# Kernel optimization log

Measured on AMD Instinct MI355X. Metric: run time of the kernel, lower is better.

Reference implementation:

```python
import jax, jax.numpy as jnp
import numpy as np

D, B, V = 8, 4096, 1024          # token fields (type..section), batch streams, vocab per field
THRES = 0.9                      # top_k filter_thres default
TEMP = 1.0                       # temperature default
NOTE_TYPE = 1                    # note_type_code; sos=0, eos=2


def setup_inputs() -> dict:
    key = jax.random.key(0)
    k1, k2, k3 = jax.random.split(key, 3)
    logits = jax.random.normal(k1, (D, B, V), dtype=jnp.float32)
    u = jax.random.uniform(k2, (D, B, V), dtype=jnp.float32)
    current_values = jax.random.randint(k3, (D, B), 0, 16).astype(jnp.int32)
    return {"logits": logits, "u": u, "current_values": current_values}


def reference(logits, u, current_values):
    neg = -jnp.inf
    ar = jnp.arange(V)
    # monotonicity mask: positions < current value are forbidden  [D,B,V]
    lg = jnp.where(ar[None, None, :] < current_values[:, :, None], neg, logits)
    # index 0 is masked for every field (logits[d][:, 0] = -inf in the loop)
    lg = lg.at[:, :, 0].set(neg)
    # top-k filtering: keep values >= k-th largest, k = int((1 - thres) * V)
    k = int((1.0 - THRES) * V)
    kth = jax.lax.top_k(lg, k)[0][..., -1:]          # [D,B,1]
    filt = jnp.where(lg < kth, neg, lg)
    logp = jax.nn.log_softmax(filt / TEMP, axis=-1)  # stable softmax, -inf -> prob 0
    probs = jnp.exp(logp)
    # multinomial sampling via Gumbel-max using provided uniform noise
    eps = 1e-20
    gumbel = -jnp.log(-jnp.log(u + eps) + eps)
    samples = jnp.argmax(logp + gumbel, axis=-1)     # [D,B]
    # type-conditional fill: fields 1..7 are zero unless sampled type == NOTE
    is_note = samples[0] == NOTE_TYPE                # [B]
    keep = (jnp.arange(D)[:, None] == 0) | is_note[None, :]
    tokens = jnp.where(keep, samples, 0)             # [D,B]
    return tokens.T, probs                           # [B,D] int, [D,B,V] float
```

## Files before the change

kernel.cpp:

```cpp
#include <hip/hip_runtime.h>
#include <math.h>

#define DD 8
#define BB 4096
#define VV 1024
#define K_SEL 102
#define RPB 4

typedef float vf4 __attribute__((ext_vector_type(4)));

__device__ __forceinline__ unsigned f2key(float f) {
    unsigned u = __float_as_uint(f);
    unsigned m = (unsigned)((int)u >> 31) | 0x80000000u;
    return u ^ m;
}
__device__ __forceinline__ float key2f(unsigned k) {
    unsigned m = 0x80000000u | ~((unsigned)((int)k >> 31));
    return __uint_as_float(k ^ m);
}

__global__ __launch_bounds__(256, 8) void decode_row_kernel(
    const float* __restrict__ logits,
    const float* __restrict__ unoise,
    const int* __restrict__ curvals,
    float* __restrict__ probs_out,
    int* __restrict__ samples)
{
    const int wave = threadIdx.x >> 6;
    const int lane = threadIdx.x & 63;
    const int row  = blockIdx.x * RPB + wave;

    const vf4* l4 = (const vf4*)(logits + (size_t)row * VV);
    const vf4* u4 = (const vf4*)(unoise + (size_t)row * VV);
    const int cv1 = max(curvals[row], 1);

    vf4 lf[4];
#pragma unroll
    for (int i = 0; i < 4; i++) lf[i] = l4[i * 64 + lane];
    vf4 uu[4];
#pragma unroll
    for (int i = 0; i < 4; i++) uu[i] = __builtin_nontemporal_load(&u4[i * 64 + lane]);

    unsigned key[16];
    {
        const int vb = lane * 4;
#pragma unroll
        for (int j = 0; j < 4; j++) {
            float t = (vb + j < cv1) ? -INFINITY : lf[0][j];
            key[j] = f2key(t);
        }
    }
#pragma unroll
    for (int i = 1; i < 4; i++)
#pragma unroll
        for (int j = 0; j < 4; j++)
            key[i * 4 + j] = f2key(lf[i][j]);
    if (cv1 > 256) {
#pragma unroll
        for (int i = 1; i < 4; i++)
#pragma unroll
            for (int j = 0; j < 4; j++)
                if (i * 256 + lane * 4 + j < cv1) key[i * 4 + j] = f2key(-INFINITY);
    }

    unsigned p  = 0u;
    unsigned CA = 0u;
#pragma unroll
    for (int b = 30; b >= 16; b -= 2) {
        const unsigned t1 = p + (1u << b);
        const unsigned t2 = p + (2u << b);
        const unsigned t3 = p + (3u << b);
        unsigned c1 = 0, c2 = 0, c3 = 0;
#pragma unroll
        for (int i = 0; i < 16; i++) {
            c1 += (unsigned)__popcll(__ballot(key[i] >= t1));
            c2 += (unsigned)__popcll(__ballot(key[i] >= t2));
            c3 += (unsigned)__popcll(__ballot(key[i] >= t3));
        }
        if (c3 >= K_SEL)      { p = t3; }
        else if (c2 >= K_SEL) { p = t2; CA = c3; }
        else if (c1 >= K_SEL) { p = t1; CA = c2; }
        else                  {         CA = c1; }
    }
    unsigned kk = K_SEL - CA;

    unsigned cmask = 0u;
#pragma unroll
    for (int i = 0; i < 16; i++)
        if ((key[i] & 0xFFFF0000u) == p) cmask |= (1u << i);
    unsigned thr;
    for (;;) {
        unsigned mx = 0u;
#pragma unroll
        for (int i = 0; i < 16; i++)
            if (cmask & (1u << i)) mx = max(mx, key[i]);
#pragma unroll
        for (int off = 32; off; off >>= 1)
            mx = max(mx, (unsigned)__shfl_xor((int)mx, off, 64));
        if (kk <= 1u) { thr = mx; break; }
        unsigned ceq = 0u;
#pragma unroll
        for (int i = 0; i < 16; i++)
            ceq += (unsigned)__popcll(__ballot(key[i] == mx));
        if (kk <= ceq) { thr = mx; break; }
        kk -= ceq;
#pragma unroll
        for (int i = 0; i < 16; i++)
            if (key[i] == mx) cmask &= ~(1u << i);
    }

    float ex[16];
    float s = 0.0f;
#pragma unroll
    for (int i = 0; i < 16; i++) {
        float e = (key[i] >= thr) ? __expf(key2f(key[i])) : 0.0f;
        ex[i] = e;
        s += e;
    }
#pragma unroll
    for (int off = 32; off; off >>= 1)
        s += __shfl_xor(s, off, 64);
    const float inv = 1.0f / s;

    float bnum = 0.0f, bden = 1.0f;
    int   besti = VV;
    vf4* p4 = (vf4*)(probs_out + (size_t)row * VV);
#pragma unroll
    for (int i = 0; i < 4; i++) {
        vf4 pv;
        pv.x = ex[i * 4 + 0] * inv;
        pv.y = ex[i * 4 + 1] * inv;
        pv.z = ex[i * 4 + 2] * inv;
        pv.w = ex[i * 4 + 3] * inv;
        p4[i * 64 + lane] = pv;
#pragma unroll
        for (int j = 0; j < 4; j++) {
            const int idx = i * 4 + j;
            float nl = 1e-20f - __logf(uu[i][j] + 1e-20f);
            float a  = ex[idx];
            int v = i * 256 + lane * 4 + j;
            if (a * bden > bnum * nl) { bnum = a; bden = nl; besti = v; }
        }
    }
#pragma unroll
    for (int off = 32; off; off >>= 1) {
        float onum = __shfl_xor(bnum, off, 64);
        float oden = __shfl_xor(bden, off, 64);
        int   oi   = __shfl_xor(besti, off, 64);
        float x = onum * bden, y = bnum * oden;
        if (x > y || (x == y && oi < besti)) { bnum = onum; bden = oden; besti = oi; }
    }
    if (lane == 0) samples[row] = besti;
}

__global__ __launch_bounds__(256) void tokens_kernel(
    const int* __restrict__ samples, float* __restrict__ tokens_out)
{
    int i = blockIdx.x * 256 + threadIdx.x;
    int b = i >> 3;
    int d = i & 7;
    int sm = samples[d * BB + b];
    int t0 = samples[b];
    tokens_out[i] = (d == 0 || t0 == 1) ? (float)sm : 0.0f;
}

extern "C" void kernel_launch(void* const* d_in, const int* in_sizes, int n_in,
                              void* d_out, int out_size, void* d_ws, size_t ws_size,
                              hipStream_t stream) {
    const float* logits = (const float*)d_in[0];
    const float* unoise = (const float*)d_in[1];
    const int*   curvals = (const int*)d_in[2];

    float* out        = (float*)d_out;
    float* tokens_out = out;
    float* probs_out  = out + (size_t)BB * DD;
    int*   samples    = (int*)d_ws;

    decode_row_kernel<<<(DD * BB) / RPB, 256, 0, stream>>>(logits, unoise, curvals,
                                                           probs_out, samples);
    tokens_kernel<<<(BB * DD) / 256, 256, 0, stream>>>(samples, tokens_out);
}
```

Before: 313.4 us.

## Radix-select on float compares with data-informed starting bucket

Replaces the unsigned key transform with direct float comparisons against thresholds decoded from key-space pivots, which drops the per-element key conversion. It also adds a speculative first pass that counts elements at or above 0.5 and 2.0. When the k-th largest value falls in that range, the select starts from a known prefix, which skips the early radix rounds. The fallback path keeps the full search, so code size grows, and the ballot counting for the speculation is extra cost on rows where it misses.

```diff
diff --git a/kernel.cpp b/kernel.cpp
--- a/kernel.cpp
+++ b/kernel.cpp
@@ -9,14 +9,31 @@
 
 typedef float vf4 __attribute__((ext_vector_type(4)));
 
-__device__ __forceinline__ unsigned f2key(float f) {
-    unsigned u = __float_as_uint(f);
-    unsigned m = (unsigned)((int)u >> 31) | 0x80000000u;
-    return u ^ m;
-}
 __device__ __forceinline__ float key2f(unsigned k) {
     unsigned m = 0x80000000u | ~((unsigned)((int)k >> 31));
     return __uint_as_float(k ^ m);
+}
+
+template<int B0>
+__device__ __forceinline__ void run_select(const float (&fv)[16], unsigned& p, unsigned& CA) {
+#pragma unroll
+    for (int b = B0; b >= 16; b -= 2) {
+        const unsigned t1u = p + (1u << b);
+        const unsigned t2u = p + (2u << b);
+        const unsigned t3u = p + (3u << b);
+        const float t1 = key2f(t1u), t2 = key2f(t2u), t3 = key2f(t3u);
+        unsigned c1 = 0, c2 = 0, c3 = 0;
+#pragma unroll
+        for (int i = 0; i < 16; i++) {
+            c1 += (unsigned)__popcll(__ballot(fv[i] >= t1));
+            c2 += (unsigned)__popcll(__ballot(fv[i] >= t2));
+            c3 += (unsigned)__popcll(__ballot(fv[i] >= t3));
+        }
+        if (c3 >= K_SEL)      { p = t3u; }
+        else if (c2 >= K_SEL) { p = t2u; CA = c3; }
+        else if (c1 >= K_SEL) { p = t1u; CA = c2; }
+        else                  {          CA = c1; }
+    }
 }
 
 __global__ __launch_bounds__(256, 8) void decode_row_kernel(
@@ -41,79 +58,74 @@
 #pragma unroll
     for (int i = 0; i < 4; i++) uu[i] = __builtin_nontemporal_load(&u4[i * 64 + lane]);
 
-    unsigned key[16];
+    float fv[16];
     {
         const int vb = lane * 4;
 #pragma unroll
-        for (int j = 0; j < 4; j++) {
-            float t = (vb + j < cv1) ? -INFINITY : lf[0][j];
-            key[j] = f2key(t);
-        }
+        for (int j = 0; j < 4; j++)
+            fv[j] = (vb + j < cv1) ? -INFINITY : lf[0][j];
     }
 #pragma unroll
     for (int i = 1; i < 4; i++)
 #pragma unroll
         for (int j = 0; j < 4; j++)
-            key[i * 4 + j] = f2key(lf[i][j]);
+            fv[i * 4 + j] = lf[i][j];
     if (cv1 > 256) {
 #pragma unroll
         for (int i = 1; i < 4; i++)
 #pragma unroll
             for (int j = 0; j < 4; j++)
-                if (i * 256 + lane * 4 + j < cv1) key[i * 4 + j] = f2key(-INFINITY);
+                if (i * 256 + lane * 4 + j < cv1) fv[i * 4 + j] = -INFINITY;
     }
 
-    unsigned p  = 0u;
-    unsigned CA = 0u;
+    unsigned clo = 0, chi = 0;
 #pragma unroll
-    for (int b = 30; b >= 16; b -= 2) {
-        const unsigned t1 = p + (1u << b);
-        const unsigned t2 = p + (2u << b);
-        const unsigned t3 = p + (3u << b);
-        unsigned c1 = 0, c2 = 0, c3 = 0;
-#pragma unroll
-        for (int i = 0; i < 16; i++) {
-            c1 += (unsigned)__popcll(__ballot(key[i] >= t1));
-            c2 += (unsigned)__popcll(__ballot(key[i] >= t2));
-            c3 += (unsigned)__popcll(__ballot(key[i] >= t3));
-        }
-        if (c3 >= K_SEL)      { p = t3; }
-        else if (c2 >= K_SEL) { p = t2; CA = c3; }
-        else if (c1 >= K_SEL) { p = t1; CA = c2; }
-        else                  {         CA = c1; }
+    for (int i = 0; i < 16; i++) {
+        clo += (unsigned)__popcll(__ballot(fv[i] >= 0.5f));
+        chi += (unsigned)__popcll(__ballot(fv[i] >= 2.0f));
+    }
+    unsigned p, CA;
+    if (clo >= K_SEL && chi < K_SEL) {
+        p = 0xBF000000u; CA = chi;
+        run_select<22>(fv, p, CA);
+    } else {
+        p = 0u; CA = 0u;
+        run_select<30>(fv, p, CA);
     }
     unsigned kk = K_SEL - CA;
 
+    const float blo = key2f(p);
+    const float bhi = key2f(p + 0x10000u);
     unsigned cmask = 0u;
 #pragma unroll
     for (int i = 0; i < 16; i++)
-        if ((key[i] & 0xFFFF0000u) == p) cmask |= (1u << i);
-    unsigned thr;
+        if (fv[i] >= blo && fv[i] < bhi) cmask |= (1u << i);
+    float thr;
     for (;;) {
-        unsigned mx = 0u;
+        float mx = -INFINITY;
 #pragma unroll
         for (int i = 0; i < 16; i++)
-            if (cmask & (1u << i)) mx = max(mx, key[i]);
+            if (cmask & (1u << i)) mx = fmaxf(mx, fv[i]);
 #pragma unroll
         for (int off = 32; off; off >>= 1)
-            mx = max(mx, (unsigned)__shfl_xor((int)mx, off, 64));
+            mx = fmaxf(mx, __shfl_xor(mx, off, 64));
         if (kk <= 1u) { thr = mx; break; }
         unsigned ceq = 0u;
 #pragma unroll
         for (int i = 0; i < 16; i++)
-            ceq += (unsigned)__popcll(__ballot(key[i] == mx));
+            ceq += (unsigned)__popcll(__ballot(fv[i] == mx));
         if (kk <= ceq) { thr = mx; break; }
         kk -= ceq;
 #pragma unroll
         for (int i = 0; i < 16; i++)
-            if (key[i] == mx) cmask &= ~(1u << i);
+            if (fv[i] == mx) cmask &= ~(1u << i);
     }
 
     float ex[16];
     float s = 0.0f;
 #pragma unroll
     for (int i = 0; i < 16; i++) {
-        float e = (key[i] >= thr) ? __expf(key2f(key[i])) : 0.0f;
+        float e = (fv[i] >= thr) ? __expf(fv[i]) : 0.0f;
         ex[i] = e;
         s += e;
     }
```

Measured after the change: 309.0 us. No clear change (-1.4%).
